# Kernel tuning notes

Measured on AMD Instinct MI355X. Metric: run time of the kernel, lower is better.

## Reference

```python
import jax, jax.numpy as jnp
import numpy as np

B, T, C, H = 8, 2048, 1024, 64

def setup_inputs() -> dict:
    key = jax.random.key(0)
    k1, k2, k3, k4 = jax.random.split(key, 4)
    return {
        "inputs": jax.random.normal(k1, (B, T, C), dtype=jnp.float32),
        "Wq": jax.random.normal(k2, (C, H), dtype=jnp.float32) * (C ** -0.5),
        "Wk": jax.random.normal(k3, (C, H), dtype=jnp.float32) * (C ** -0.5),
        "Wv": jax.random.normal(k4, (C, H), dtype=jnp.float32) * (C ** -0.5),
    }

def reference(inputs, Wq, Wk, Wv):
    # q,k,v: [B,T,H]
    q = jnp.einsum('btc,ch->bth', inputs, Wq)
    k = jnp.einsum('btc,ch->bth', inputs, Wk)
    v = jnp.einsum('btc,ch->bth', inputs, Wv)
    c = inputs.shape[-1]
    # NOTE: original scales by C**-0.5 (embedding dim), not head_size**-0.5
    scale = jnp.asarray(c, inputs.dtype) ** -0.5
    wei = jnp.einsum('bqh,bkh->bqk', q, k) * scale  # [B,T,T]
    t = inputs.shape[1]
    causal = jnp.tril(jnp.ones((t, t), dtype=bool))
    wei = jnp.where(causal[None, :, :], wei, -jnp.inf)
    wei = jax.nn.softmax(wei, axis=-1)
    # dropout is identity in eval / DROP_RATE=0
    out = jnp.einsum('bqk,bkh->bqh', wei, v)  # [B,T,H]
    return out
```

## Files before the change

kernel.cpp:

```cpp
#include <hip/hip_runtime.h>
#include <stdint.h>

#define B_ 8
#define T_ 2048
#define C_ 1024
#define H_ 64
#define M_ (B_*T_)

typedef __bf16 bf16x8 __attribute__((ext_vector_type(8)));
typedef float  f32x4  __attribute__((ext_vector_type(4)));

union U4B { uint4 u; bf16x8 v; };

__device__ __forceinline__ unsigned short f32_to_bf16(float f) {
    union { float f; uint32_t u; } c; c.f = f;
    uint32_t u = c.u;
    u += 0x7fffu + ((u >> 16) & 1u);
    return (unsigned short)(u >> 16);
}
__device__ __forceinline__ uint32_t pack2_bf16(float a, float b) {
    return (uint32_t)f32_to_bf16(a) | ((uint32_t)f32_to_bf16(b) << 16);
}

__global__ __launch_bounds__(256) void prepack_w(const float* __restrict__ Wq,
        const float* __restrict__ Wk, const float* __restrict__ Wv,
        unsigned short* __restrict__ wpk) {
    int o = blockIdx.x * 256 + threadIdx.x;
    if (o >= 24576) return;
    int lane = o & 63, kc = (o >> 6) & 31, nt = o >> 11;
    int l15 = lane & 15, grp = lane >> 4;
    int n = nt * 16 + l15;
    int k = kc * 32 + grp * 8;
    const float* W = (n < 64) ? Wq : (n < 128) ? Wk : Wv;
    int col = n & 63;
    unsigned short tmp[8];
    #pragma unroll
    for (int j = 0; j < 8; j++) tmp[j] = f32_to_bf16(W[(size_t)(k + j) * 64 + col]);
    *(uint4*)(wpk + (size_t)o * 8) = *(uint4*)tmp;
}

__global__ __launch_bounds__(256, 4) void qkv_kernel(const float* __restrict__ X,
        const unsigned short* __restrict__ wpk,
        unsigned short* __restrict__ qb, unsigned short* __restrict__ kb,
        unsigned short* __restrict__ vt) {
    __shared__ unsigned short Xl[16][72];
    const int tid = threadIdx.x;
    const int wave = tid >> 6, lane = tid & 63;
    const int grp = lane >> 4, l15 = lane & 15;
    const int mb = blockIdx.x * 16;
    const int srow = tid >> 4, sc4 = (tid & 15) * 4;

    f32x4 acc[3];
    for (int i = 0; i < 3; i++) acc[i] = (f32x4){0.f, 0.f, 0.f, 0.f};

    const float* xp = X + (size_t)(mb + srow) * 1024 + sc4;
    uint4 wr[2][6];
    #pragma unroll
    for (int jj = 0; jj < 3; jj++) {
        int nt = wave * 3 + jj;
        const uint4* wb = (const uint4*)(wpk + ((size_t)(nt * 32) * 64 + lane) * 8);
        wr[0][jj * 2]     = wb[0];
        wr[0][jj * 2 + 1] = wb[64];
    }
    float4 xf = *(const float4*)xp;

    for (int it = 0; it < 16; it++) {
        const int cur = it & 1, nxt = cur ^ 1;
        *(uint2*)&Xl[srow][sc4] = (uint2){ pack2_bf16(xf.x, xf.y), pack2_bf16(xf.z, xf.w) };
        __syncthreads();
        if (it < 15) {
            xf = *(const float4*)(xp + (it + 1) * 64);
            #pragma unroll
            for (int jj = 0; jj < 3; jj++) {
                int nt = wave * 3 + jj;
                const uint4* wb = (const uint4*)(wpk + ((size_t)(nt * 32 + (it + 1) * 2) * 64 + lane) * 8);
                wr[nxt][jj * 2]     = wb[0];
                wr[nxt][jj * 2 + 1] = wb[64];
            }
        }
        bf16x8 a0 = *(const bf16x8*)&Xl[l15][grp * 8];
        bf16x8 a1 = *(const bf16x8*)&Xl[l15][32 + grp * 8];
        #pragma unroll
        for (int jj = 0; jj < 3; jj++) {
            U4B b0, b1; b0.u = wr[cur][jj * 2]; b1.u = wr[cur][jj * 2 + 1];
            acc[jj] = __builtin_amdgcn_mfma_f32_16x16x32_bf16(a0, b0.v, acc[jj], 0, 0, 0);
            acc[jj] = __builtin_amdgcn_mfma_f32_16x16x32_bf16(a1, b1.v, acc[jj], 0, 0, 0);
        }
        __syncthreads();
    }
    const int r0 = mb + grp * 4;
    const int bb = mb >> 11;
    const int t0 = (mb + grp * 4) & 2047;
    #pragma unroll
    for (int jj = 0; jj < 3; jj++) {
        int col = (wave * 3 + jj) * 16 + l15;
        if (col < 64) {
            for (int r = 0; r < 4; r++)
                qb[(size_t)(r0 + r) * 64 + col] = f32_to_bf16(acc[jj][r] * 0.03125f);
        } else if (col < 128) {
            for (int r = 0; r < 4; r++)
                kb[(size_t)(r0 + r) * 64 + (col - 64)] = f32_to_bf16(acc[jj][r]);
        } else {
            int c = col - 128;
            ushort4 vv;
            vv.x = f32_to_bf16(acc[jj][0]); vv.y = f32_to_bf16(acc[jj][1]);
            vv.z = f32_to_bf16(acc[jj][2]); vv.w = f32_to_bf16(acc[jj][3]);
            *(ushort4*)(vt + ((size_t)bb * 64 + c) * 2048 + t0) = vv;
        }
    }
}

__global__ __launch_bounds__(256) void attn1_kernel(const unsigned short* __restrict__ qb,
        const unsigned short* __restrict__ kb, const unsigned short* __restrict__ vt,
        float* __restrict__ pm, float* __restrict__ pl, float* __restrict__ pacc) {
    __shared__ unsigned short Kl[2][64][72];
    __shared__ unsigned short Vl[2][64][72];
    const int tid = threadIdx.x;
    const int wave = tid >> 6, lane = tid & 63;
    const int grp = lane >> 4, l15 = lane & 15;
    const int b = blockIdx.x & 7;
    const int f = blockIdx.x >> 3;
    int s, j;
    if (f < 32)      { s = 0; j = 31 - f; }
    else if (f < 56) { s = 1; j = 31 - (f - 32); }
    else if (f < 72) { s = 2; j = 31 - (f - 56); }
    else             { s = 3; j = 31 - (f - 72); }
    const int qbase = j * 64 + wave * 16;
    const int ktend = min(8, j + 1 - 8 * s);

    const unsigned short* qp = qb + ((size_t)b * 2048 + qbase + l15) * 64 + grp * 8;
    bf16x8 bq0 = *(const bf16x8*)qp;
    bf16x8 bq1 = *(const bf16x8*)(qp + 32);

    float m_i = -1e30f, l_i = 0.f;
    f32x4 acc[4];
    for (int d = 0; d < 4; d++) acc[d] = (f32x4){0.f, 0.f, 0.f, 0.f};

    const unsigned short* kB = kb + ((size_t)b * 2048 + s * 512) * 64;
    const unsigned short* vB = vt + (size_t)b * 64 * 2048 + s * 512;
    const int r1 = tid >> 3, c1 = (tid & 7) * 8;
    const int r2 = (tid + 256) >> 3, c2 = c1;

    uint4 kr0, kr1, vr0, vr1;
    kr0 = *(const uint4*)(kB + (size_t)r1 * 64 + c1);
    kr1 = *(const uint4*)(kB + (size_t)r2 * 64 + c2);
    vr0 = *(const uint4*)(vB + (size_t)r1 * 2048 + c1);
    vr1 = *(const uint4*)(vB + (size_t)r2 * 2048 + c2);
    *(uint4*)&Kl[0][r1][c1] = kr0;  *(uint4*)&Kl[0][r2][c2] = kr1;
    *(uint4*)&Vl[0][r1][c1] = vr0;  *(uint4*)&Vl[0][r2][c2] = vr1;
    __syncthreads();

    for (int kt = 0; kt < ktend; kt++) {
        const int buf = kt & 1;
        const bool more = (kt + 1) < ktend;
        if (more) {
            const unsigned short* kN = kB + (size_t)(kt + 1) * 64 * 64;
            const unsigned short* vN = vB + (kt + 1) * 64;
            kr0 = *(const uint4*)(kN + (size_t)r1 * 64 + c1);
            kr1 = *(const uint4*)(kN + (size_t)r2 * 64 + c2);
            vr0 = *(const uint4*)(vN + (size_t)r1 * 2048 + c1);
            vr1 = *(const uint4*)(vN + (size_t)r2 * 2048 + c2);
        }
        const int keybase = s * 512 + kt * 64;
        f32x4 st[4];
        #pragma unroll
        for (int nt = 0; nt < 4; nt++) {
            bf16x8 a0 = *(const bf16x8*)&Kl[buf][nt * 16 + l15][grp * 8];
            bf16x8 a1 = *(const bf16x8*)&Kl[buf][nt * 16 + l15][32 + grp * 8];
            f32x4 t = (f32x4){0.f, 0.f, 0.f, 0.f};
            t = __builtin_amdgcn_mfma_f32_16x16x32_bf16(a0, bq0, t, 0, 0, 0);
            t = __builtin_amdgcn_mfma_f32_16x16x32_bf16(a1, bq1, t, 0, 0, 0);
            st[nt] = t;
        }
        if (keybase + 63 > qbase) {
            int q = qbase + l15;
            #pragma unroll
            for (int nt = 0; nt < 4; nt++)
                for (int r = 0; r < 4; r++)
                    if (keybase + nt * 16 + grp * 4 + r > q) st[nt][r] = -1e30f;
        }
        float tmax = -1e30f;
        #pragma unroll
        for (int nt = 0; nt < 4; nt++)
            for (int r = 0; r < 4; r++) tmax = fmaxf(tmax, st[nt][r]);
        tmax = fmaxf(tmax, __shfl_xor(tmax, 16, 64));
        tmax = fmaxf(tmax, __shfl_xor(tmax, 32, 64));
        float mnew = fmaxf(m_i, tmax);
        float alpha = __expf(m_i - mnew);
        m_i = mnew;
        float p[4][4]; float ts = 0.f;
        #pragma unroll
        for (int nt = 0; nt < 4; nt++)
            for (int r = 0; r < 4; r++) { p[nt][r] = __expf(st[nt][r] - mnew); ts += p[nt][r]; }
        ts += __shfl_xor(ts, 16, 64);
        ts += __shfl_xor(ts, 32, 64);
        l_i = l_i * alpha + ts;
        #pragma unroll
        for (int d = 0; d < 4; d++) acc[d] *= alpha;
        uint32_t t0a = pack2_bf16(p[0][0], p[0][1]), t0b = pack2_bf16(p[0][2], p[0][3]);
        uint32_t t1a = pack2_bf16(p[1][0], p[1][1]), t1b = pack2_bf16(p[1][2], p[1][3]);
        uint32_t t2a = pack2_bf16(p[2][0], p[2][1]), t2b = pack2_bf16(p[2][2], p[2][3]);
        uint32_t t3a = pack2_bf16(p[3][0], p[3][1]), t3b = pack2_bf16(p[3][2], p[3][3]);
        const int s0l = ((grp & 1) << 5) + l15, s1l = s0l + 16;
        const bool hi = (grp >= 2);
        U4B bw0, bw1;
        {
            uint32_t e0a = (uint32_t)__shfl((int)t0a, s0l, 64);
            uint32_t e0b = (uint32_t)__shfl((int)t0b, s0l, 64);
            uint32_t e0c = (uint32_t)__shfl((int)t0a, s1l, 64);
            uint32_t e0d = (uint32_t)__shfl((int)t0b, s1l, 64);
            uint32_t e1a = (uint32_t)__shfl((int)t1a, s0l, 64);
            uint32_t e1b = (uint32_t)__shfl((int)t1b, s0l, 64);
            uint32_t e1c = (uint32_t)__shfl((int)t1a, s1l, 64);
            uint32_t e1d = (uint32_t)__shfl((int)t1b, s1l, 64);
            bw0.u = (uint4){ hi ? e1a : e0a, hi ? e1b : e0b, hi ? e1c : e0c, hi ? e1d : e0d };
        }
        {
            uint32_t e0a = (uint32_t)__shfl((int)t2a, s0l, 64);
            uint32_t e0b = (uint32_t)__shfl((int)t2b, s0l, 64);
            uint32_t e0c = (uint32_t)__shfl((int)t2a, s1l, 64);
            uint32_t e0d = (uint32_t)__shfl((int)t2b, s1l, 64);
            uint32_t e1a = (uint32_t)__shfl((int)t3a, s0l, 64);
            uint32_t e1b = (uint32_t)__shfl((int)t3b, s0l, 64);
            uint32_t e1c = (uint32_t)__shfl((int)t3a, s1l, 64);
            uint32_t e1d = (uint32_t)__shfl((int)t3b, s1l, 64);
            bw1.u = (uint4){ hi ? e1a : e0a, hi ? e1b : e0b, hi ? e1c : e0c, hi ? e1d : e0d };
        }
        #pragma unroll
        for (int dt = 0; dt < 4; dt++) {
            bf16x8 av0 = *(const bf16x8*)&Vl[buf][dt * 16 + l15][grp * 8];
            bf16x8 av1 = *(const bf16x8*)&Vl[buf][dt * 16 + l15][32 + grp * 8];
            acc[dt] = __builtin_amdgcn_mfma_f32_16x16x32_bf16(av0, bw0.v, acc[dt], 0, 0, 0);
            acc[dt] = __builtin_amdgcn_mfma_f32_16x16x32_bf16(av1, bw1.v, acc[dt], 0, 0, 0);
        }
        if (more) {
            const int nb = buf ^ 1;
            *(uint4*)&Kl[nb][r1][c1] = kr0;  *(uint4*)&Kl[nb][r2][c2] = kr1;
            *(uint4*)&Vl[nb][r1][c1] = vr0;  *(uint4*)&Vl[nb][r2][c2] = vr1;
        }
        __syncthreads();
    }
    size_t rowq = (size_t)b * 2048 + qbase + l15;
    size_t p = rowq * 4 + s;
    if (grp == 0) { pm[p] = m_i; pl[p] = l_i; }
    #pragma unroll
    for (int dt = 0; dt < 4; dt++)
        *(f32x4*)&pacc[p * 64 + dt * 16 + grp * 4] = acc[dt];
}

__global__ __launch_bounds__(256) void attn2_kernel(const float* __restrict__ pm,
        const float* __restrict__ pl, const float* __restrict__ pacc,
        float* __restrict__ out) {
    int idx = blockIdx.x * 256 + threadIdx.x;
    int row = idx >> 4;
    int d0 = (idx & 15) * 4;
    int t = row & 2047;
    int ns = (t >> 9) + 1;
    float mv[4];
    float M = -1e30f;
    for (int s = 0; s < ns; s++) { mv[s] = pm[(size_t)row * 4 + s]; M = fmaxf(M, mv[s]); }
    float den = 0.f;
    f32x4 num = (f32x4){0.f, 0.f, 0.f, 0.f};
    for (int s = 0; s < ns; s++) {
        float w = __expf(mv[s] - M);
        den += w * pl[(size_t)row * 4 + s];
        f32x4 a = *(const f32x4*)&pacc[((size_t)row * 4 + s) * 64 + d0];
        num += w * a;
    }
    float inv = 1.f / den;
    *(f32x4*)&out[(size_t)row * 64 + d0] = num * inv;
}

extern "C" void kernel_launch(void* const* d_in, const int* in_sizes, int n_in,
                              void* d_out, int out_size, void* d_ws, size_t ws_size,
                              hipStream_t stream) {
    const float* X  = (const float*)d_in[0];
    const float* Wq = (const float*)d_in[1];
    const float* Wk = (const float*)d_in[2];
    const float* Wv = (const float*)d_in[3];
    float* out = (float*)d_out;

    unsigned short* qb  = (unsigned short*)d_ws;
    unsigned short* kb  = qb + (size_t)M_ * 64;
    unsigned short* wpk = kb + (size_t)M_ * 64;
    unsigned short* vt  = wpk + (size_t)24576 * 8;
    float* pm   = (float*)(vt + (size_t)B_ * 64 * 2048);
    float* pl   = pm + (size_t)M_ * 4;
    float* pacc = pl + (size_t)M_ * 4;

    prepack_w<<<96, 256, 0, stream>>>(Wq, Wk, Wv, wpk);
    qkv_kernel<<<1024, 256, 0, stream>>>(X, wpk, qb, kb, vt);
    attn1_kernel<<<640, 256, 0, stream>>>(qb, kb, vt, pm, pl, pacc);
    attn2_kernel<<<1024, 256, 0, stream>>>(pm, pl, pacc, out);
}
```

Measured before the change: 146.4 us.

## Enlarge QKV projection tile, stage weights in LDS, single-buffer attention K/V

```diff
diff --git a/kernel.cpp b/kernel.cpp
--- a/kernel.cpp
+++ b/kernel.cpp
@@ -19,7 +19,14 @@
     return (unsigned short)(u >> 16);
 }
 __device__ __forceinline__ uint32_t pack2_bf16(float a, float b) {
+#if __has_builtin(__builtin_amdgcn_cvt_pk_bf16_f32)
+    typedef __bf16 bf16x2 __attribute__((ext_vector_type(2)));
+    union { bf16x2 v; uint32_t u; } c;
+    c.v = __builtin_amdgcn_cvt_pk_bf16_f32(a, b);
+    return c.u;
+#else
     return (uint32_t)f32_to_bf16(a) | ((uint32_t)f32_to_bf16(b) << 16);
+#endif
 }
 
 __global__ __launch_bounds__(256) void prepack_w(const float* __restrict__ Wq,
@@ -27,7 +34,7 @@
         unsigned short* __restrict__ wpk) {
     int o = blockIdx.x * 256 + threadIdx.x;
     if (o >= 24576) return;
-    int lane = o & 63, kc = (o >> 6) & 31, nt = o >> 11;
+    int lane = o & 63, nt = (o >> 6) % 12, kc = o / (64 * 12);
     int l15 = lane & 15, grp = lane >> 4;
     int n = nt * 16 + l15;
     int k = kc * 32 + grp * 8;
@@ -39,73 +46,94 @@
     *(uint4*)(wpk + (size_t)o * 8) = *(uint4*)tmp;
 }
 
-__global__ __launch_bounds__(256, 4) void qkv_kernel(const float* __restrict__ X,
+__global__ __launch_bounds__(256) void qkv_kernel(const float* __restrict__ X,
         const unsigned short* __restrict__ wpk,
         unsigned short* __restrict__ qb, unsigned short* __restrict__ kb,
         unsigned short* __restrict__ vt) {
-    __shared__ unsigned short Xl[16][72];
+    __shared__ unsigned short Xl[2][64][40];
+    __shared__ unsigned short Wl[2][4][3][64][8];
     const int tid = threadIdx.x;
     const int wave = tid >> 6, lane = tid & 63;
     const int grp = lane >> 4, l15 = lane & 15;
-    const int mb = blockIdx.x * 16;
-    const int srow = tid >> 4, sc4 = (tid & 15) * 4;
-
-    f32x4 acc[3];
-    for (int i = 0; i < 3; i++) acc[i] = (f32x4){0.f, 0.f, 0.f, 0.f};
-
-    const float* xp = X + (size_t)(mb + srow) * 1024 + sc4;
-    uint4 wr[2][6];
-    #pragma unroll
-    for (int jj = 0; jj < 3; jj++) {
-        int nt = wave * 3 + jj;
-        const uint4* wb = (const uint4*)(wpk + ((size_t)(nt * 32) * 64 + lane) * 8);
-        wr[0][jj * 2]     = wb[0];
-        wr[0][jj * 2 + 1] = wb[64];
-    }
-    float4 xf = *(const float4*)xp;
-
-    for (int it = 0; it < 16; it++) {
+    const int mb = blockIdx.x * 64;
+
+    f32x4 acc[4][3];
+    #pragma unroll
+    for (int i = 0; i < 4; i++)
+        for (int j = 0; j < 3; j++) acc[i][j] = (f32x4){0.f, 0.f, 0.f, 0.f};
+
+    const int srow = tid >> 2, sk = (tid & 3) * 8;
+    const float* xp = X + (size_t)(mb + srow) * 1024 + sk;
+
+    float4 f0 = *(const float4*)(xp);
+    float4 f1 = *(const float4*)(xp + 4);
+    uint4 wr[3];
+    #pragma unroll
+    for (int jj = 0; jj < 3; jj++)
+        wr[jj] = *(const uint4*)(wpk + ((size_t)(0 * 12 + wave * 3 + jj) * 64 + lane) * 8);
+    {
+        uint4 xu = { pack2_bf16(f0.x, f0.y), pack2_bf16(f0.z, f0.w),
+                     pack2_bf16(f1.x, f1.y), pack2_bf16(f1.z, f1.w) };
+        *(uint4*)&Xl[0][srow][sk] = xu;
+        #pragma unroll
+        for (int jj = 0; jj < 3; jj++)
+            *(uint4*)&Wl[0][wave][jj][lane][0] = wr[jj];
+    }
+    __syncthreads();
+
+    for (int it = 0; it < 32; it++) {
         const int cur = it & 1, nxt = cur ^ 1;
-        *(uint2*)&Xl[srow][sc4] = (uint2){ pack2_bf16(xf.x, xf.y), pack2_bf16(xf.z, xf.w) };
+        if (it < 31) {
+            const int kn = (it + 1) * 32;
+            f0 = *(const float4*)(xp + kn);
+            f1 = *(const float4*)(xp + kn + 4);
+            #pragma unroll
+            for (int jj = 0; jj < 3; jj++)
+                wr[jj] = *(const uint4*)(wpk + ((size_t)((it + 1) * 12 + wave * 3 + jj) * 64 + lane) * 8);
+        }
+        bf16x8 bfr[3];
+        #pragma unroll
+        for (int jj = 0; jj < 3; jj++)
+            bfr[jj] = *(const bf16x8*)&Wl[cur][wave][jj][lane][0];
+        #pragma unroll
+        for (int i = 0; i < 4; i++) {
+            bf16x8 a = *(const bf16x8*)&Xl[cur][i * 16 + l15][grp * 8];
+            #pragma unroll
+            for (int jj = 0; jj < 3; jj++)
+                acc[i][jj] = __builtin_amdgcn_mfma_f32_16x16x32_bf16(a, bfr[jj], acc[i][jj], 0, 0, 0);
+        }
+        if (it < 31) {
+            uint4 xu = { pack2_bf16(f0.x, f0.y), pack2_bf16(f0.z, f0.w),
+                         pack2_bf16(f1.x, f1.y), pack2_bf16(f1.z, f1.w) };
+            *(uint4*)&Xl[nxt][srow][sk] = xu;
+            #pragma unroll
+            for (int jj = 0; jj < 3; jj++)
+                *(uint4*)&Wl[nxt][wave][jj][lane][0] = wr[jj];
+        }
         __syncthreads();
-        if (it < 15) {
-            xf = *(const float4*)(xp + (it + 1) * 64);
-            #pragma unroll
-            for (int jj = 0; jj < 3; jj++) {
-                int nt = wave * 3 + jj;
-                const uint4* wb = (const uint4*)(wpk + ((size_t)(nt * 32 + (it + 1) * 2) * 64 + lane) * 8);
-                wr[nxt][jj * 2]     = wb[0];
-                wr[nxt][jj * 2 + 1] = wb[64];
-            }
-        }
-        bf16x8 a0 = *(const bf16x8*)&Xl[l15][grp * 8];
-        bf16x8 a1 = *(const bf16x8*)&Xl[l15][32 + grp * 8];
-        #pragma unroll
-        for (int jj = 0; jj < 3; jj++) {
-            U4B b0, b1; b0.u = wr[cur][jj * 2]; b1.u = wr[cur][jj * 2 + 1];
-            acc[jj] = __builtin_amdgcn_mfma_f32_16x16x32_bf16(a0, b0.v, acc[jj], 0, 0, 0);
-            acc[jj] = __builtin_amdgcn_mfma_f32_16x16x32_bf16(a1, b1.v, acc[jj], 0, 0, 0);
-        }
-        __syncthreads();
-    }
-    const int r0 = mb + grp * 4;
+    }
+
     const int bb = mb >> 11;
-    const int t0 = (mb + grp * 4) & 2047;
     #pragma unroll
     for (int jj = 0; jj < 3; jj++) {
         int col = (wave * 3 + jj) * 16 + l15;
-        if (col < 64) {
-            for (int r = 0; r < 4; r++)
-                qb[(size_t)(r0 + r) * 64 + col] = f32_to_bf16(acc[jj][r] * 0.03125f);
-        } else if (col < 128) {
-            for (int r = 0; r < 4; r++)
-                kb[(size_t)(r0 + r) * 64 + (col - 64)] = f32_to_bf16(acc[jj][r]);
-        } else {
-            int c = col - 128;
-            ushort4 vv;
-            vv.x = f32_to_bf16(acc[jj][0]); vv.y = f32_to_bf16(acc[jj][1]);
-            vv.z = f32_to_bf16(acc[jj][2]); vv.w = f32_to_bf16(acc[jj][3]);
-            *(ushort4*)(vt + ((size_t)bb * 64 + c) * 2048 + t0) = vv;
+        #pragma unroll
+        for (int i = 0; i < 4; i++) {
+            int r0 = mb + i * 16 + grp * 4;
+            if (col < 64) {
+                for (int r = 0; r < 4; r++)
+                    qb[(size_t)(r0 + r) * 64 + col] = f32_to_bf16(acc[i][jj][r] * 0.03125f);
+            } else if (col < 128) {
+                for (int r = 0; r < 4; r++)
+                    kb[(size_t)(r0 + r) * 64 + (col - 64)] = f32_to_bf16(acc[i][jj][r]);
+            } else {
+                int c = col - 128;
+                int t0 = r0 & 2047;
+                ushort4 vv;
+                vv.x = f32_to_bf16(acc[i][jj][0]); vv.y = f32_to_bf16(acc[i][jj][1]);
+                vv.z = f32_to_bf16(acc[i][jj][2]); vv.w = f32_to_bf16(acc[i][jj][3]);
+                *(ushort4*)(vt + ((size_t)bb * 64 + c) * 2048 + t0) = vv;
+            }
         }
     }
 }
@@ -113,8 +141,8 @@
 __global__ __launch_bounds__(256) void attn1_kernel(const unsigned short* __restrict__ qb,
         const unsigned short* __restrict__ kb, const unsigned short* __restrict__ vt,
         float* __restrict__ pm, float* __restrict__ pl, float* __restrict__ pacc) {
-    __shared__ unsigned short Kl[2][64][72];
-    __shared__ unsigned short Vl[2][64][72];
+    __shared__ unsigned short Kl[64][72];
+    __shared__ unsigned short Vl[64][72];
     const int tid = threadIdx.x;
     const int wave = tid >> 6, lane = tid & 63;
     const int grp = lane >> 4, l15 = lane & 15;
@@ -146,14 +174,12 @@
     kr1 = *(const uint4*)(kB + (size_t)r2 * 64 + c2);
     vr0 = *(const uint4*)(vB + (size_t)r1 * 2048 + c1);
     vr1 = *(const uint4*)(vB + (size_t)r2 * 2048 + c2);
-    *(uint4*)&Kl[0][r1][c1] = kr0;  *(uint4*)&Kl[0][r2][c2] = kr1;
-    *(uint4*)&Vl[0][r1][c1] = vr0;  *(uint4*)&Vl[0][r2][c2] = vr1;
-    __syncthreads();
 
     for (int kt = 0; kt < ktend; kt++) {
-        const int buf = kt & 1;
-        const bool more = (kt + 1) < ktend;
-        if (more) {
+        *(uint4*)&Kl[r1][c1] = kr0;  *(uint4*)&Kl[r2][c2] = kr1;
+        *(uint4*)&Vl[r1][c1] = vr0;  *(uint4*)&Vl[r2][c2] = vr1;
+        __syncthreads();
+        if (kt + 1 < ktend) {
             const unsigned short* kN = kB + (size_t)(kt + 1) * 64 * 64;
             const unsigned short* vN = vB + (kt + 1) * 64;
             kr0 = *(const uint4*)(kN + (size_t)r1 * 64 + c1);
@@ -165,8 +191,8 @@
         f32x4 st[4];
         #pragma unroll
         for (int nt = 0; nt < 4; nt++) {
-            bf16x8 a0 = *(const bf16x8*)&Kl[buf][nt * 16 + l15][grp * 8];
-            bf16x8 a1 = *(const bf16x8*)&Kl[buf][nt * 16 + l15][32 + grp * 8];
+            bf16x8 a0 = *(const bf16x8*)&Kl[nt * 16 + l15][grp * 8];
+            bf16x8 a1 = *(const bf16x8*)&Kl[nt * 16 + l15][32 + grp * 8];
             f32x4 t = (f32x4){0.f, 0.f, 0.f, 0.f};
             t = __builtin_amdgcn_mfma_f32_16x16x32_bf16(a0, bq0, t, 0, 0, 0);
             t = __builtin_amdgcn_mfma_f32_16x16x32_bf16(a1, bq1, t, 0, 0, 0);
@@ -228,15 +254,10 @@
         }
         #pragma unroll
         for (int dt = 0; dt < 4; dt++) {
-            bf16x8 av0 = *(const bf16x8*)&Vl[buf][dt * 16 + l15][grp * 8];
-            bf16x8 av1 = *(const bf16x8*)&Vl[buf][dt * 16 + l15][32 + grp * 8];
+            bf16x8 av0 = *(const bf16x8*)&Vl[dt * 16 + l15][grp * 8];
+            bf16x8 av1 = *(const bf16x8*)&Vl[dt * 16 + l15][32 + grp * 8];
             acc[dt] = __builtin_amdgcn_mfma_f32_16x16x32_bf16(av0, bw0.v, acc[dt], 0, 0, 0);
             acc[dt] = __builtin_amdgcn_mfma_f32_16x16x32_bf16(av1, bw1.v, acc[dt], 0, 0, 0);
-        }
-        if (more) {
-            const int nb = buf ^ 1;
-            *(uint4*)&Kl[nb][r1][c1] = kr0;  *(uint4*)&Kl[nb][r2][c2] = kr1;
-            *(uint4*)&Vl[nb][r1][c1] = vr0;  *(uint4*)&Vl[nb][r2][c2] = vr1;
         }
         __syncthreads();
     }
@@ -289,7 +310,7 @@
     float* pacc = pl + (size_t)M_ * 4;
 
     prepack_w<<<96, 256, 0, stream>>>(Wq, Wk, Wv, wpk);
-    qkv_kernel<<<1024, 256, 0, stream>>>(X, wpk, qb, kb, vt);
+    qkv_kernel<<<256, 256, 0, stream>>>(X, wpk, qb, kb, vt);
     attn1_kernel<<<640, 256, 0, stream>>>(qb, kb, vt, pm, pl, pacc);
     attn2_kernel<<<1024, 256, 0, stream>>>(pm, pl, pacc, out);
 }
```

Result: no change. 148.7 us (+1.6%).
